# Kernel tuning notes

Measured on AMD Instinct MI355X. Metric: run time of the kernel, lower is better.

## Reference

```python
import jax, jax.numpy as jnp
import numpy as np

D = 512
DB = D // 4          # 128
R = 4                # window radius
KB = 9               # boundary kernel
DH = D // 2          # attn mlp hidden
VOCABS = {"quality": 64, "root": 13, "bass": 13, "key": 25}
COMPS = ["quality", "root", "bass", "key"]
B, T = 4, 4096


def _ln(x, g, b, eps=1e-5):
    mu = jnp.mean(x, axis=-1, keepdims=True)
    var = jnp.var(x, axis=-1, keepdims=True)
    return (x - mu) * jax.lax.rsqrt(var + eps) * g + b


def setup_inputs() -> dict:
    key = jax.random.key(0)
    ks = jax.random.split(key, 24)
    s = 0.02
    inp = {
        "h": jax.random.normal(ks[0], (B, T, D), jnp.float32),
        # boundary head
        "w_bnd": jax.random.normal(ks[1], (D,), jnp.float32) * s,
        "b_bnd": jnp.zeros((1,), jnp.float32),
        # boundary smoother conv1d(1,1,KB)
        "conv_k": jax.random.normal(ks[2], (KB,), jnp.float32) * s,
        "conv_b": jnp.zeros((1,), jnp.float32),
        # FiLM boundary embeddings
        "e0": jnp.zeros((DB,), jnp.float32),
        "e1": jax.random.normal(ks[3], (DB,), jnp.float32) * s,
        # LayerNorms
        "ln_in_g": jnp.ones((D + DB,), jnp.float32),
        "ln_in_b": jnp.zeros((D + DB,), jnp.float32),
        "ln_h_g": jnp.ones((D,), jnp.float32),
        "ln_h_b": jnp.zeros((D,), jnp.float32),
        # FiLM mlp
        "film_w": jax.random.normal(ks[4], (D + DB, 2 * D), jnp.float32) * s,
        "film_b": jnp.zeros((2 * D,), jnp.float32),
        # per-component attn MLP (stacked over 4 comps)
        "attn_w1": jax.random.normal(ks[5], (4, D, DH), jnp.float32) * s,
        "attn_b1": jnp.zeros((4, DH), jnp.float32),
        "attn_w2": jax.random.normal(ks[6], (4, DH), jnp.float32) * s,
        "attn_b2": jnp.zeros((4,), jnp.float32),
        # per-component projector first layer (stacked)
        "proj_w1": jax.random.normal(ks[7], (4, D, D), jnp.float32) * s,
        "proj_b1": jnp.zeros((4, D), jnp.float32),
    }
    for i, c in enumerate(COMPS):
        inp[f"proj_w2_{c[0]}" if c != "key" else "proj_w2_k"] = jax.random.normal(ks[8 + i], (D, VOCABS[c]), jnp.float32) * s
        inp[f"proj_b2_{c[0]}" if c != "key" else "proj_b2_k"] = jnp.zeros((VOCABS[c],), jnp.float32)
    return inp


def reference(h, w_bnd, b_bnd, conv_k, conv_b, e0, e1,
              ln_in_g, ln_in_b, ln_h_g, ln_h_b, film_w, film_b,
              attn_w1, attn_b1, attn_w2, attn_b2, proj_w1, proj_b1,
              proj_w2_q, proj_b2_q, proj_w2_r, proj_b2_r,
              proj_w2_b, proj_b2_b, proj_w2_k, proj_b2_k):
    Bz, Tz, Dz = h.shape
    # boundary head + smoothing (conv1d, same padding) + sigmoid
    bl = jnp.einsum("btd,d->bt", h, w_bnd) + b_bnd[0]            # [B,T]
    sm = jax.lax.conv_general_dilated(bl[:, None, :], conv_k[None, None, :],
                                      (1,), [(KB // 2, KB // 2)]) + conv_b[0]
    b_soft = jax.nn.sigmoid(sm[:, 0, :])                          # [B,T]
    # FiLM
    eb = b_soft[..., None] * e1 + (1.0 - b_soft[..., None]) * e0  # [B,T,DB]
    film_in = _ln(jnp.concatenate([h, eb], axis=-1), ln_in_g, ln_in_b)
    gb = film_in @ film_w + film_b                                # [B,T,2D]
    gamma, beta = gb[..., :Dz], gb[..., Dz:]
    z = _ln(h, ln_h_g, ln_h_b) * (1.0 + gamma) + beta             # [B,T,D]
    # local windows via replicate pad + gather
    hp = jnp.pad(h, ((0, 0), (R, R), (0, 0)), mode="edge")        # [B,T+2R,D]
    idx = jnp.arange(Tz)[:, None] + jnp.arange(2 * R + 1)[None, :]  # [T,W]
    local = hp[:, idx, :]                                         # [B,T,W,D]
    c = jnp.concatenate([z[:, :, None, :], local], axis=2)        # [B,T,C,D]
    # attention pooling for all 4 components at once
    s1 = jax.nn.gelu(jnp.einsum("btcd,kdh->kbtch", c, attn_w1)
                     + attn_b1[:, None, None, None, :], approximate=False)
    scores = jnp.einsum("kbtch,kh->kbtc", s1, attn_w2) + attn_b2[:, None, None, None]
    attn = jax.nn.softmax(scores, axis=-1)                        # [K,B,T,C]
    pooled = jnp.einsum("kbtc,btcd->kbtd", attn, c)               # [K,B,T,D]
    p1 = jax.nn.gelu(jnp.einsum("kbtd,kde->kbte", pooled, proj_w1)
                     + proj_b1[:, None, None, :], approximate=False)
    lq = p1[0] @ proj_w2_q + proj_b2_q
    lr = p1[1] @ proj_w2_r + proj_b2_r
    lb = p1[2] @ proj_w2_b + proj_b2_b
    lk = p1[3] @ proj_w2_k + proj_b2_k
    return jnp.concatenate([lq, lr, lb, lk, bl[..., None]], axis=-1)  # [B,T,116]
```

## Files before the change

### kernel.cpp

```cpp
#include <hip/hip_runtime.h>
#include <hip/hip_bf16.h>

typedef unsigned short u16;
typedef unsigned int u32;

#define NR 16384
#define TT 4096

typedef __bf16 bf16_t;
typedef bf16_t bf16x8 __attribute__((ext_vector_type(8)));
typedef float f32x4 __attribute__((ext_vector_type(4)));

__device__ __forceinline__ float b2f(u16 u){ return __uint_as_float(((u32)u)<<16); }
__device__ __forceinline__ u16 f2b(float f){
  u32 u = __float_as_uint(f);
  u32 r = u + 0x7fffu + ((u>>16)&1u);
  return (u16)(r>>16);
}
__device__ __forceinline__ void up2(u32 u, float&a, float&b){
  a = __uint_as_float(u<<16);
  b = __uint_as_float(u & 0xffff0000u);
}
__device__ __forceinline__ void ld8(const u16* p, float* f){
  uint4 v = *(const uint4*)p;
  up2(v.x,f[0],f[1]); up2(v.y,f[2],f[3]);
  up2(v.z,f[4],f[5]); up2(v.w,f[6],f[7]);
}
__device__ __forceinline__ float wred(float v){
  #pragma unroll
  for(int o=32;o>0;o>>=1) v += __shfl_down(v,o,64);
  return v;
}
__device__ __forceinline__ float gelu_f(float x){
  return 0.5f*x*(1.0f+erff(x*0.7071067811865475f));
}
__device__ __forceinline__ void gl_lds(const void* g, void* l){
  __builtin_amdgcn_global_load_lds(
      (__attribute__((address_space(1))) void*)(void*)g,
      (__attribute__((address_space(3))) void*)l, 16, 0, 0);
}

__global__ void k_tw(const float* __restrict__ src, u16* __restrict__ dst,
                     int K, int N, long long sS, long long sD){
  __shared__ float t[32][33];
  const float* S = src + (size_t)blockIdx.z*sS;
  u16* D = dst + (size_t)blockIdx.z*sD;
  int k0 = blockIdx.y*32, n0 = blockIdx.x*32;
  int r = threadIdx.x>>5, c = threadIdx.x&31;
  #pragma unroll
  for(int p=0;p<4;p++) t[r+p*8][c] = S[(size_t)(k0+r+p*8)*N + n0 + c];
  __syncthreads();
  #pragma unroll
  for(int p=0;p<4;p++) D[(size_t)(n0+r+p*8)*K + k0 + c] = f2b(t[c][r+p*8]);
}

__global__ void k_wbig(const float* __restrict__ wq, const float* __restrict__ bq,
                       const float* __restrict__ wr, const float* __restrict__ br,
                       const float* __restrict__ wb_, const float* __restrict__ bb_,
                       const float* __restrict__ wk, const float* __restrict__ bk,
                       u16* __restrict__ WT, float* __restrict__ bias2){
  int c = blockIdx.x, tid = threadIdx.x;
  const float* Wm=nullptr; const float* Bm=nullptr; int k=0,j=0,V=0;
  if(c<64){k=0;j=c;V=64;Wm=wq;Bm=bq;}
  else if(c<77){k=1;j=c-64;V=13;Wm=wr;Bm=br;}
  else if(c<90){k=2;j=c-77;V=13;Wm=wb_;Bm=bb_;}
  else if(c<115){k=3;j=c-90;V=25;Wm=wk;Bm=bk;}
  for(int kk=tid;kk<2048;kk+=256){
    float v = 0.f;
    if(c<115 && (kk>>9)==k) v = Wm[(size_t)(kk&511)*V + j];
    WT[(size_t)c*2048+kk] = f2b(v);
  }
  if(tid==0) bias2[c] = (c<115) ? Bm[j] : 0.f;
}

__global__ void k_bnd(const float* __restrict__ h, const float* __restrict__ wb,
                      const float* __restrict__ bb,
                      float* __restrict__ bl, float* __restrict__ hsum, float* __restrict__ hss,
                      u16* __restrict__ hbf){
  int wave = threadIdx.x>>6, lane = threadIdx.x&63;
  int n = blockIdx.x*4 + wave;
  const float4* hp = (const float4*)(h + (size_t)n*512 + lane*8);
  const float4* wp = (const float4*)(wb + lane*8);
  float4 h0 = hp[0], h1 = hp[1], w0 = wp[0], w1 = wp[1];
  float hv[8] = {h0.x,h0.y,h0.z,h0.w,h1.x,h1.y,h1.z,h1.w};
  float wv[8] = {w0.x,w0.y,w0.z,w0.w,w1.x,w1.y,w1.z,w1.w};
  float dot=0.f, s=0.f, ss=0.f;
  #pragma unroll
  for(int i=0;i<8;i++){ dot += hv[i]*wv[i]; s += hv[i]; ss += hv[i]*hv[i]; }
  u16* hd = hbf + (size_t)n*512 + lane*8;
  *(ushort4*)hd     = make_ushort4(f2b(hv[0]),f2b(hv[1]),f2b(hv[2]),f2b(hv[3]));
  *(ushort4*)(hd+4) = make_ushort4(f2b(hv[4]),f2b(hv[5]),f2b(hv[6]),f2b(hv[7]));
  dot = wred(dot); s = wred(s); ss = wred(ss);
  if(lane==0){ bl[n] = dot + bb[0]; hsum[n]=s; hss[n]=ss; }
}

__global__ void k_conv(const float* __restrict__ bl, const float* __restrict__ ck,
                       const float* __restrict__ cb, float* __restrict__ bsoft){
  int n = blockIdx.x*256 + threadIdx.x;
  int b = n>>12, t = n&4095;
  float acc = cb[0];
  #pragma unroll
  for(int i=0;i<9;i++){
    int tt = t-4+i;
    if(tt>=0 && tt<TT) acc += bl[(b<<12)+tt]*ck[i];
  }
  bsoft[n] = 1.0f/(1.0f+expf(-acc));
}

__global__ void k_filmin(const float* __restrict__ h, const float* __restrict__ bsoft,
                         const float* __restrict__ e0, const float* __restrict__ e1,
                         const float* __restrict__ g, const float* __restrict__ bb,
                         u16* __restrict__ fin){
  __shared__ float xb[640];
  __shared__ float red[8];
  int n = blockIdx.x, tid = threadIdx.x;
  float bs = bsoft[n];
  float s=0.f, ss=0.f;
  for(int idx=tid; idx<640; idx+=256){
    float v;
    if(idx<512) v = h[(size_t)n*512+idx];
    else { int j=idx-512; v = bs*e1[j] + (1.0f-bs)*e0[j]; }
    xb[idx]=v; s+=v; ss+=v*v;
  }
  s = wred(s); ss = wred(ss);
  int wave = tid>>6, lane = tid&63;
  if(lane==0){ red[wave]=s; red[wave+4]=ss; }
  __syncthreads();
  float S = red[0]+red[1]+red[2]+red[3];
  float SS = red[4]+red[5]+red[6]+red[7];
  float mu = S*(1.0f/640.0f);
  float var = SS*(1.0f/640.0f) - mu*mu;
  float rs = rsqrtf(var + 1e-5f);
  for(int idx=tid; idx<640; idx+=256){
    float v = (xb[idx]-mu)*rs*g[idx] + bb[idx];
    fin[(size_t)n*640+idx] = f2b(v);
  }
}

template<int ACT>
__global__ __launch_bounds__(256) void k_mgemm(
    const u16* __restrict__ X, const u16* __restrict__ WT, const float* __restrict__ Bv,
    u16* __restrict__ C, int K, int Nc, int ldC,
    long long sX, long long sW, long long sB, long long sC){
  __shared__ __align__(16) u16 As[128*32];
  __shared__ __align__(16) u16 Bs[128*32];
  int tid = threadIdx.x;
  int wave = tid>>6, lane = tid&63;
  const u16* Xb = X + (size_t)blockIdx.z*sX;
  const u16* Wb = WT + (size_t)blockIdx.z*sW;
  const float* Bb = Bv + (size_t)blockIdx.z*sB;
  u16* Cb = C + (size_t)blockIdx.z*sC;
  int row0 = blockIdx.y*128, col0 = blockIdx.x*128;
  int wr = (wave>>1)*64, wc = (wave&1)*64;
  int lrow = lane>>2;
  int lcol = (lane&3)*8;
  int m15 = lane&15, q = lane>>4;
  f32x4 acc[4][4] = {};
  for(int k0=0;k0<K;k0+=32){
    const u16* ga = Xb + (size_t)(row0 + wave*32 + lrow)*K + k0 + lcol;
    u16* la = As + wave*32*32;
    gl_lds(ga, la);
    gl_lds(ga + (size_t)16*K, la + 16*32);
    const u16* gw = Wb + (size_t)(col0 + wave*32 + lrow)*K + k0 + lcol;
    u16* lb = Bs + wave*32*32;
    gl_lds(gw, lb);
    gl_lds(gw + (size_t)16*K, lb + 16*32);
    __syncthreads();
    bf16x8 af[4], bfr[4];
    #pragma unroll
    for(int i=0;i<4;i++){
      af[i]  = *(const bf16x8*)&As[(wr + i*16 + m15)*32 + q*8];
      bfr[i] = *(const bf16x8*)&Bs[(wc + i*16 + m15)*32 + q*8];
    }
    #pragma unroll
    for(int i=0;i<4;i++)
      #pragma unroll
      for(int j=0;j<4;j++)
        acc[i][j] = __builtin_amdgcn_mfma_f32_16x16x32_bf16(af[i], bfr[j], acc[i][j], 0,0,0);
    __syncthreads();
  }
  #pragma unroll
  for(int j=0;j<4;j++){
    int cg = col0 + wc + j*16 + m15;
    float bias = Bb[cg];
    #pragma unroll
    for(int i=0;i<4;i++){
      int rbase = row0 + wr + i*16 + q*4;
      #pragma unroll
      for(int r=0;r<4;r++){
        float v = acc[i][j][r] + bias;
        if(ACT) v = gelu_f(v);
        Cb[(size_t)(rbase+r)*ldC + cg] = f2b(v);
      }
    }
  }
}

__global__ __launch_bounds__(256) void k_fgemm(
    const u16* __restrict__ X2, const u16* __restrict__ WT, const float* __restrict__ bias2,
    const float* __restrict__ bl, float* __restrict__ out){
  __shared__ __align__(16) u16 As[128*32];
  __shared__ __align__(16) u16 Bs[128*32];
  int tid = threadIdx.x;
  int wave = tid>>6, lane = tid&63;
  int row0 = blockIdx.x*128;
  int wr = (wave>>1)*64, wc = (wave&1)*64;
  int lrow = lane>>2, lcol = (lane&3)*8, m15 = lane&15, q = lane>>4;
  f32x4 acc[4][4] = {};
  for(int k0=0;k0<2048;k0+=32){
    const u16* ga = X2 + (size_t)(row0 + wave*32 + lrow)*2048 + k0 + lcol;
    u16* la = As + wave*32*32;
    gl_lds(ga, la);
    gl_lds(ga + (size_t)16*2048, la + 16*32);
    const u16* gw = WT + (size_t)(wave*32 + lrow)*2048 + k0 + lcol;
    u16* lb = Bs + wave*32*32;
    gl_lds(gw, lb);
    gl_lds(gw + (size_t)16*2048, lb + 16*32);
    __syncthreads();
    bf16x8 af[4], bfr[4];
    #pragma unroll
    for(int i=0;i<4;i++){
      af[i]  = *(const bf16x8*)&As[(wr + i*16 + m15)*32 + q*8];
      bfr[i] = *(const bf16x8*)&Bs[(wc + i*16 + m15)*32 + q*8];
    }
    #pragma unroll
    for(int i=0;i<4;i++)
      #pragma unroll
      for(int j=0;j<4;j++)
        acc[i][j] = __builtin_amdgcn_mfma_f32_16x16x32_bf16(af[i], bfr[j], acc[i][j], 0,0,0);
    __syncthreads();
  }
  #pragma unroll
  for(int j=0;j<4;j++){
    int cg = wc + j*16 + m15;
    float bias = bias2[cg];
    #pragma unroll
    for(int i=0;i<4;i++){
      int rbase = row0 + wr + i*16 + q*4;
      #pragma unroll
      for(int r=0;r<4;r++){
        int rr = rbase + r;
        if(cg < 115) out[(size_t)rr*116 + cg] = acc[i][j][r] + bias;
        else if(cg == 115) out[(size_t)rr*116 + 115] = bl[rr];
      }
    }
  }
}

__global__ void k_z(const float* __restrict__ h, const float* __restrict__ hsum,
                    const float* __restrict__ hss, const float* __restrict__ g,
                    const float* __restrict__ bb, const u16* __restrict__ gb,
                    u16* __restrict__ z){
  int n = blockIdx.x, tid = threadIdx.x;
  float mu = hsum[n]*(1.0f/512.0f);
  float var = hss[n]*(1.0f/512.0f) - mu*mu;
  float rs = rsqrtf(var+1e-5f);
  for(int idx=tid; idx<512; idx+=256){
    float hv = h[(size_t)n*512+idx];
    float ln = (hv-mu)*rs*g[idx]+bb[idx];
    float gamma = b2f(gb[(size_t)n*1024+idx]);
    float beta  = b2f(gb[(size_t)n*1024+512+idx]);
    z[(size_t)n*512+idx] = f2b(ln*(1.0f+gamma)+beta);
  }
}

__global__ void k_scred(const u16* __restrict__ G, const float* __restrict__ w2,
                        const float* __restrict__ b2v, float* __restrict__ sc){
  int wave = threadIdx.x>>6, lane = threadIdx.x&63;
  int n = blockIdx.x*4 + wave;
  int k = blockIdx.y;
  uint2 gv = *(const uint2*)(G + ((size_t)k*NR + n)*256 + lane*4);
  float4 wv = *(const float4*)(w2 + k*256 + lane*4);
  float a0,a1,a2,a3;
  up2(gv.x,a0,a1); up2(gv.y,a2,a3);
  float s = a0*wv.x+a1*wv.y+a2*wv.z+a3*wv.w;
  s = wred(s);
  if(lane==0) sc[(size_t)k*NR+n] = s + b2v[k];
}

__global__ __launch_bounds__(256) void k_pool(
    const u16* __restrict__ hb, const u16* __restrict__ z,
    const float* __restrict__ sch, const float* __restrict__ scz,
    u16* __restrict__ P){
  int wave = threadIdx.x>>6, lane = threadIdx.x&63;
  int n = blockIdx.x*4 + wave;
  int b = n>>12, t = n&4095;
  int k = lane&3, j = lane>>2;
  float s;
  if(j==0) s = scz[(size_t)k*NR+n];
  else if(j<10){
    int tc = t-5+j; tc = tc<0?0:(tc>TT-1?TT-1:tc);
    s = sch[(size_t)k*NR + (b<<12) + tc];
  } else s = -1e30f;
  float m = s;
  #pragma unroll
  for(int o=4;o<64;o<<=1) m = fmaxf(m, __shfl_xor(m,o,64));
  float e = (j<10)? expf(s-m) : 0.f;
  float sum = e;
  #pragma unroll
  for(int o=4;o<64;o<<=1) sum += __shfl_xor(sum,o,64);
  float ev = e/sum;
  int d0 = lane*8;
  float acc[4][8] = {};
  #pragma unroll
  for(int jj=0;jj<10;jj++){
    const u16* src;
    if(jj==0) src = z + (size_t)n*512 + d0;
    else {
      int tc = t-5+jj; tc = tc<0?0:(tc>TT-1?TT-1:tc);
      src = hb + ((size_t)(b<<12)+tc)*512 + d0;
    }
    float f[8]; ld8(src, f);
    float w0 = __shfl(ev, jj*4+0, 64);
    float w1 = __shfl(ev, jj*4+1, 64);
    float w2 = __shfl(ev, jj*4+2, 64);
    float w3 = __shfl(ev, jj*4+3, 64);
    #pragma unroll
    for(int i=0;i<8;i++){
      acc[0][i] += w0*f[i];
      acc[1][i] += w1*f[i];
      acc[2][i] += w2*f[i];
      acc[3][i] += w3*f[i];
    }
  }
  #pragma unroll
  for(int kk=0;kk<4;kk++){
    u16* dst = P + ((size_t)kk*NR + n)*512 + d0;
    *(ushort4*)dst     = make_ushort4(f2b(acc[kk][0]),f2b(acc[kk][1]),f2b(acc[kk][2]),f2b(acc[kk][3]));
    *(ushort4*)(dst+4) = make_ushort4(f2b(acc[kk][4]),f2b(acc[kk][5]),f2b(acc[kk][6]),f2b(acc[kk][7]));
  }
}

#define OFF_BL     0u
#define OFF_BSOFT  65536u
#define OFF_HSUM   131072u
#define OFF_HSS    196608u
#define OFF_SCH    262144u
#define OFF_SCZ    524288u
#define OFF_FIN    786432u
#define OFF_GB     21757952u
#define OFF_Z      55312384u
#define OFF_HBF    72089600u
#define OFF_WF     88866816u
#define OFF_WA     90177536u
#define OFF_WP     91226112u
#define OFF_P      93323264u
#define OFF_WB     160432128u
#define OFF_B2     160956416u

extern "C" void kernel_launch(void* const* d_in, const int* in_sizes, int n_in,
                              void* d_out, int out_size, void* d_ws, size_t ws_size,
                              hipStream_t stream){
  const float* h       = (const float*)d_in[0];
  const float* w_bnd   = (const float*)d_in[1];
  const float* b_bnd   = (const float*)d_in[2];
  const float* conv_k  = (const float*)d_in[3];
  const float* conv_b  = (const float*)d_in[4];
  const float* e0      = (const float*)d_in[5];
  const float* e1      = (const float*)d_in[6];
  const float* ln_in_g = (const float*)d_in[7];
  const float* ln_in_b = (const float*)d_in[8];
  const float* ln_h_g  = (const float*)d_in[9];
  const float* ln_h_b  = (const float*)d_in[10];
  const float* film_w  = (const float*)d_in[11];
  const float* film_b  = (const float*)d_in[12];
  const float* attn_w1 = (const float*)d_in[13];
  const float* attn_b1 = (const float*)d_in[14];
  const float* attn_w2 = (const float*)d_in[15];
  const float* attn_b2 = (const float*)d_in[16];
  const float* proj_w1 = (const float*)d_in[17];
  const float* proj_b1 = (const float*)d_in[18];
  const float* wq = (const float*)d_in[19];
  const float* bq = (const float*)d_in[20];
  const float* wr = (const float*)d_in[21];
  const float* br = (const float*)d_in[22];
  const float* wb_ = (const float*)d_in[23];
  const float* bb_ = (const float*)d_in[24];
  const float* wk = (const float*)d_in[25];
  const float* bk = (const float*)d_in[26];
  float* out = (float*)d_out;
  char* ws = (char*)d_ws;

  float* bl    = (float*)(ws + OFF_BL);
  float* bsoft = (float*)(ws + OFF_BSOFT);
  float* hsum  = (float*)(ws + OFF_HSUM);
  float* hss   = (float*)(ws + OFF_HSS);
  float* sch   = (float*)(ws + OFF_SCH);
  float* scz   = (float*)(ws + OFF_SCZ);
  u16* fin     = (u16*)(ws + OFF_FIN);
  u16* X2      = (u16*)(ws + OFF_FIN);
  u16* gb      = (u16*)(ws + OFF_GB);
  u16* z       = (u16*)(ws + OFF_Z);
  u16* hbf     = (u16*)(ws + OFF_HBF);
  u16* wfilm   = (u16*)(ws + OFF_WF);
  u16* wattn   = (u16*)(ws + OFF_WA);
  u16* wproj   = (u16*)(ws + OFF_WP);
  u16* P       = (u16*)(ws + OFF_P);
  u16* G       = P;
  u16* wbig    = (u16*)(ws + OFF_WB);
  float* bias2 = (float*)(ws + OFF_B2);

  {
    dim3 g(1024/32, 640/32, 1);
    k_tw<<<g,256,0,stream>>>(film_w, wfilm, 640, 1024, 0, 0);
  }
  {
    dim3 g(256/32, 512/32, 4);
    k_tw<<<g,256,0,stream>>>(attn_w1, wattn, 512, 256, 512LL*256, 256LL*512);
  }
  {
    dim3 g(512/32, 512/32, 4);
    k_tw<<<g,256,0,stream>>>(proj_w1, wproj, 512, 512, 512LL*512, 512LL*512);
  }
  k_wbig<<<128,256,0,stream>>>(wq,bq,wr,br,wb_,bb_,wk,bk, wbig, bias2);

  k_bnd<<<NR/4,256,0,stream>>>(h,w_bnd,b_bnd,bl,hsum,hss,hbf);
  k_conv<<<NR/256,256,0,stream>>>(bl,conv_k,conv_b,bsoft);
  k_filmin<<<NR,256,0,stream>>>(h,bsoft,e0,e1,ln_in_g,ln_in_b,fin);

  dim3 gFilm(1024/128, NR/128, 1);
  k_mgemm<0><<<gFilm,256,0,stream>>>(fin, wfilm, film_b, gb, 640, 1024, 1024, 0,0,0,0);

  k_z<<<NR,256,0,stream>>>(h,hsum,hss,ln_h_g,ln_h_b,gb,z);

  dim3 gSc(256/128, NR/128, 4);
  dim3 gRed(NR/4, 4);
  k_mgemm<1><<<gSc,256,0,stream>>>(hbf, wattn, attn_b1, G, 512, 256, 256,
                                   0, 256LL*512, 256, (long long)NR*256);
  k_scred<<<gRed,256,0,stream>>>(G, attn_w2, attn_b2, sch);
  k_mgemm<1><<<gSc,256,0,stream>>>(z, wattn, attn_b1, G, 512, 256, 256,
                                   0, 256LL*512, 256, (long long)NR*256);
  k_scred<<<gRed,256,0,stream>>>(G, attn_w2, attn_b2, scz);

  k_pool<<<NR/4,256,0,stream>>>(hbf,z,sch,scz,P);

  dim3 gP(512/128, NR/128, 4);
  k_mgemm<1><<<gP,256,0,stream>>>(P, wproj, proj_b1, X2, 512, 512, 2048,
                                  (long long)NR*512, 512LL*512, 512, 512);

  k_fgemm<<<NR/128,256,0,stream>>>(X2, wbig, bias2, bl, out);
}
```

Before: 472.6 us.

## Replace block-diagonal final GEMM with per-component GEMMs and vectorize mgemm epilogue

The final projection GEMM previously multiplied against a 2048-wide block-diagonal weight matrix that was mostly zeros. It is now split into five small GEMMs, one per 32-column slice of each component, and each reads only its 512-wide slice of X2, which removes the zero-block multiplies. The boundary logit is written to the output directly from the boundary kernel. The generic mgemm swaps its MFMA operands so each lane holds four consecutive columns, allowing a float4 bias load and a 4-wide bf16 store in the epilogue. The trade-off is more blocks with small tiles and A reloaded for each component slice.

```diff
diff --git a/kernel.cpp b/kernel.cpp
--- a/kernel.cpp
+++ b/kernel.cpp
@@ -54,29 +54,29 @@
   for(int p=0;p<4;p++) D[(size_t)(n0+r+p*8)*K + k0 + c] = f2b(t[c][r+p*8]);
 }
 
-__global__ void k_wbig(const float* __restrict__ wq, const float* __restrict__ bq,
-                       const float* __restrict__ wr, const float* __restrict__ br,
-                       const float* __restrict__ wb_, const float* __restrict__ bb_,
-                       const float* __restrict__ wk, const float* __restrict__ bk,
-                       u16* __restrict__ WT, float* __restrict__ bias2){
-  int c = blockIdx.x, tid = threadIdx.x;
-  const float* Wm=nullptr; const float* Bm=nullptr; int k=0,j=0,V=0;
-  if(c<64){k=0;j=c;V=64;Wm=wq;Bm=bq;}
-  else if(c<77){k=1;j=c-64;V=13;Wm=wr;Bm=br;}
-  else if(c<90){k=2;j=c-77;V=13;Wm=wb_;Bm=bb_;}
-  else if(c<115){k=3;j=c-90;V=25;Wm=wk;Bm=bk;}
-  for(int kk=tid;kk<2048;kk+=256){
-    float v = 0.f;
-    if(c<115 && (kk>>9)==k) v = Wm[(size_t)(kk&511)*V + j];
-    WT[(size_t)c*2048+kk] = f2b(v);
-  }
-  if(tid==0) bias2[c] = (c<115) ? Bm[j] : 0.f;
+__global__ void k_w2c(const float* __restrict__ wq, const float* __restrict__ bq,
+                      const float* __restrict__ wr, const float* __restrict__ br,
+                      const float* __restrict__ wb_, const float* __restrict__ bb_,
+                      const float* __restrict__ wk, const float* __restrict__ bk,
+                      u16* __restrict__ W2c, float* __restrict__ b2c){
+  int idx = blockIdx.x;
+  int p = idx>>5, j = idx&31, tid = threadIdx.x;
+  const float* Wm; const float* Bm; int V; int cofs = 0;
+  if(p<=1){ Wm=wq; Bm=bq; V=64; cofs = p*32; }
+  else if(p==2){ Wm=wr; Bm=br; V=13; }
+  else if(p==3){ Wm=wb_; Bm=bb_; V=13; }
+  else { Wm=wk; Bm=bk; V=25; }
+  int c = j + cofs;
+  bool valid = c < V;
+  for(int k=tid;k<512;k+=256)
+    W2c[(size_t)idx*512 + k] = f2b(valid ? Wm[(size_t)k*V + c] : 0.f);
+  if(tid==0) b2c[idx] = valid ? Bm[c] : 0.f;
 }
 
 __global__ void k_bnd(const float* __restrict__ h, const float* __restrict__ wb,
                       const float* __restrict__ bb,
                       float* __restrict__ bl, float* __restrict__ hsum, float* __restrict__ hss,
-                      u16* __restrict__ hbf){
+                      u16* __restrict__ hbf, float* __restrict__ out){
   int wave = threadIdx.x>>6, lane = threadIdx.x&63;
   int n = blockIdx.x*4 + wave;
   const float4* hp = (const float4*)(h + (size_t)n*512 + lane*8);
@@ -91,7 +91,11 @@
   *(ushort4*)hd     = make_ushort4(f2b(hv[0]),f2b(hv[1]),f2b(hv[2]),f2b(hv[3]));
   *(ushort4*)(hd+4) = make_ushort4(f2b(hv[4]),f2b(hv[5]),f2b(hv[6]),f2b(hv[7]));
   dot = wred(dot); s = wred(s); ss = wred(ss);
-  if(lane==0){ bl[n] = dot + bb[0]; hsum[n]=s; hss[n]=ss; }
+  if(lane==0){
+    float v = dot + bb[0];
+    bl[n] = v; hsum[n]=s; hss[n]=ss;
+    out[(size_t)n*116 + 115] = v;
+  }
 }
 
 __global__ void k_conv(const float* __restrict__ bl, const float* __restrict__ ck,
@@ -176,72 +180,70 @@
     for(int i=0;i<4;i++)
       #pragma unroll
       for(int j=0;j<4;j++)
-        acc[i][j] = __builtin_amdgcn_mfma_f32_16x16x32_bf16(af[i], bfr[j], acc[i][j], 0,0,0);
+        acc[i][j] = __builtin_amdgcn_mfma_f32_16x16x32_bf16(bfr[j], af[i], acc[i][j], 0,0,0);
     __syncthreads();
   }
   #pragma unroll
-  for(int j=0;j<4;j++){
-    int cg = col0 + wc + j*16 + m15;
-    float bias = Bb[cg];
-    #pragma unroll
-    for(int i=0;i<4;i++){
-      int rbase = row0 + wr + i*16 + q*4;
-      #pragma unroll
-      for(int r=0;r<4;r++){
-        float v = acc[i][j][r] + bias;
-        if(ACT) v = gelu_f(v);
-        Cb[(size_t)(rbase+r)*ldC + cg] = f2b(v);
-      }
-    }
-  }
-}
-
-__global__ __launch_bounds__(256) void k_fgemm(
-    const u16* __restrict__ X2, const u16* __restrict__ WT, const float* __restrict__ bias2,
-    const float* __restrict__ bl, float* __restrict__ out){
+  for(int i=0;i<4;i++){
+    size_t mrow = (size_t)(row0 + wr + i*16 + m15)*ldC;
+    #pragma unroll
+    for(int j=0;j<4;j++){
+      int n0 = col0 + wc + j*16 + q*4;
+      float4 bias = *(const float4*)&Bb[n0];
+      float v0 = acc[i][j][0] + bias.x;
+      float v1 = acc[i][j][1] + bias.y;
+      float v2 = acc[i][j][2] + bias.z;
+      float v3 = acc[i][j][3] + bias.w;
+      if(ACT){ v0=gelu_f(v0); v1=gelu_f(v1); v2=gelu_f(v2); v3=gelu_f(v3); }
+      *(ushort4*)(Cb + mrow + n0) = make_ushort4(f2b(v0),f2b(v1),f2b(v2),f2b(v3));
+    }
+  }
+}
+
+__global__ __launch_bounds__(256) void k_f2(
+    const u16* __restrict__ X2, const u16* __restrict__ W2c, const float* __restrict__ b2c,
+    float* __restrict__ out){
   __shared__ __align__(16) u16 As[128*32];
-  __shared__ __align__(16) u16 Bs[128*32];
-  int tid = threadIdx.x;
-  int wave = tid>>6, lane = tid&63;
-  int row0 = blockIdx.x*128;
-  int wr = (wave>>1)*64, wc = (wave&1)*64;
+  __shared__ __align__(16) u16 Bs[32*32];
+  int tid = threadIdx.x, wave = tid>>6, lane = tid&63;
+  int row0 = blockIdx.x*128, p = blockIdx.y;
+  int hk = (p<=1)?0:(p-1);
+  int B0 = (p==0)?0:(p==1)?32:(p==2)?64:(p==3)?77:90;
+  int V  = (p<=1)?32:(p==4)?25:13;
   int lrow = lane>>2, lcol = (lane&3)*8, m15 = lane&15, q = lane>>4;
-  f32x4 acc[4][4] = {};
-  for(int k0=0;k0<2048;k0+=32){
-    const u16* ga = X2 + (size_t)(row0 + wave*32 + lrow)*2048 + k0 + lcol;
+  f32x4 acc[2][2] = {};
+  for(int k0=0;k0<512;k0+=32){
+    const u16* ga = X2 + (size_t)(row0 + wave*32 + lrow)*2048 + hk*512 + k0 + lcol;
     u16* la = As + wave*32*32;
     gl_lds(ga, la);
     gl_lds(ga + (size_t)16*2048, la + 16*32);
-    const u16* gw = WT + (size_t)(wave*32 + lrow)*2048 + k0 + lcol;
-    u16* lb = Bs + wave*32*32;
-    gl_lds(gw, lb);
-    gl_lds(gw + (size_t)16*2048, lb + 16*32);
+    if(wave<2){
+      const u16* gw = W2c + (size_t)(p*32 + wave*16 + lrow)*512 + k0 + lcol;
+      gl_lds(gw, Bs + wave*16*32);
+    }
     __syncthreads();
-    bf16x8 af[4], bfr[4];
-    #pragma unroll
-    for(int i=0;i<4;i++){
-      af[i]  = *(const bf16x8*)&As[(wr + i*16 + m15)*32 + q*8];
-      bfr[i] = *(const bf16x8*)&Bs[(wc + i*16 + m15)*32 + q*8];
-    }
-    #pragma unroll
-    for(int i=0;i<4;i++)
+    bf16x8 af[2], bfr[2];
+    #pragma unroll
+    for(int i=0;i<2;i++) af[i] = *(const bf16x8*)&As[(wave*32 + i*16 + m15)*32 + q*8];
+    #pragma unroll
+    for(int j=0;j<2;j++) bfr[j] = *(const bf16x8*)&Bs[(j*16+m15)*32 + q*8];
+    #pragma unroll
+    for(int i=0;i<2;i++)
       #pragma unroll
-      for(int j=0;j<4;j++)
-        acc[i][j] = __builtin_amdgcn_mfma_f32_16x16x32_bf16(af[i], bfr[j], acc[i][j], 0,0,0);
+      for(int j=0;j<2;j++)
+        acc[i][j] = __builtin_amdgcn_mfma_f32_16x16x32_bf16(bfr[j], af[i], acc[i][j], 0,0,0);
     __syncthreads();
   }
   #pragma unroll
-  for(int j=0;j<4;j++){
-    int cg = wc + j*16 + m15;
-    float bias = bias2[cg];
-    #pragma unroll
-    for(int i=0;i<4;i++){
-      int rbase = row0 + wr + i*16 + q*4;
+  for(int i=0;i<2;i++){
+    size_t mrow = (size_t)(row0 + wave*32 + i*16 + m15)*116;
+    #pragma unroll
+    for(int j=0;j<2;j++){
+      int nl0 = j*16 + q*4;
       #pragma unroll
       for(int r=0;r<4;r++){
-        int rr = rbase + r;
-        if(cg < 115) out[(size_t)rr*116 + cg] = acc[i][j][r] + bias;
-        else if(cg == 115) out[(size_t)rr*116 + 115] = bl[rr];
+        int nl = nl0 + r;
+        if(nl < V) out[mrow + B0 + nl] = acc[i][j][r] + b2c[p*32+nl];
       }
     }
   }
@@ -345,8 +347,8 @@
 #define OFF_WA     90177536u
 #define OFF_WP     91226112u
 #define OFF_P      93323264u
-#define OFF_WB     160432128u
-#define OFF_B2     160956416u
+#define OFF_W2C    160432128u
+#define OFF_B2C    160595968u
 
 extern "C" void kernel_launch(void* const* d_in, const int* in_sizes, int n_in,
                               void* d_out, int out_size, void* d_ws, size_t ws_size,
@@ -397,8 +399,8 @@
   u16* wproj   = (u16*)(ws + OFF_WP);
   u16* P       = (u16*)(ws + OFF_P);
   u16* G       = P;
-  u16* wbig    = (u16*)(ws + OFF_WB);
-  float* bias2 = (float*)(ws + OFF_B2);
+  u16* w2c     = (u16*)(ws + OFF_W2C);
+  float* b2c   = (float*)(ws + OFF_B2C);
 
   {
     dim3 g(1024/32, 640/32, 1);
@@ -412,9 +414,9 @@
     dim3 g(512/32, 512/32, 4);
     k_tw<<<g,256,0,stream>>>(proj_w1, wproj, 512, 512, 512LL*512, 512LL*512);
   }
-  k_wbig<<<128,256,0,stream>>>(wq,bq,wr,br,wb_,bb_,wk,bk, wbig, bias2);
-
-  k_bnd<<<NR/4,256,0,stream>>>(h,w_bnd,b_bnd,bl,hsum,hss,hbf);
+  k_w2c<<<160,256,0,stream>>>(wq,bq,wr,br,wb_,bb_,wk,bk, w2c, b2c);
+
+  k_bnd<<<NR/4,256,0,stream>>>(h,w_bnd,b_bnd,bl,hsum,hss,hbf,out);
   k_conv<<<NR/256,256,0,stream>>>(bl,conv_k,conv_b,bsoft);
   k_filmin<<<NR,256,0,stream>>>(h,bsoft,e0,e1,ln_in_g,ln_in_b,fin);
 
@@ -438,5 +440,6 @@
   k_mgemm<1><<<gP,256,0,stream>>>(P, wproj, proj_b1, X2, 512, 512, 2048,
                                   (long long)NR*512, 512LL*512, 512, 512);
 
-  k_fgemm<<<NR/128,256,0,stream>>>(X2, wbig, bias2, bl, out);
-}
+  dim3 gF(NR/128, 5);
+  k_f2<<<gF,256,0,stream>>>(X2, w2c, b2c, out);
+}
```

After: 444.6 us. 5.9% less time.
